# Performance work log

Measured on AMD Instinct MI355X. Metric: run time of the kernel, lower is better.

## Reference

```python
import jax, jax.numpy as jnp
import numpy as np

HIDDEN = 1024
HEADS = 12
HEAD_DIM = 64
NEG = -1e12


def _rope(x):
    # x: [B, N, H, d], rotate along seq axis (axis 1), interleaved pairs
    B, N, H, d = x.shape
    inv_freq = 1.0 / (10000.0 ** (jnp.arange(0, d, 2, dtype=jnp.float32) / d))  # [d/2]
    pos = jnp.arange(N, dtype=jnp.float32)
    ang = pos[:, None] * inv_freq[None, :]                 # [N, d/2]
    sin = jnp.repeat(jnp.sin(ang), 2, axis=-1)[None, :, None, :]  # [1,N,1,d]
    cos = jnp.repeat(jnp.cos(ang), 2, axis=-1)[None, :, None, :]
    even = x[..., ::2]
    odd = x[..., 1::2]
    rot = jnp.stack([-odd, even], axis=-1).reshape(B, N, H, d)
    return x * cos + rot * sin


def setup_inputs() -> dict:
    key = jax.random.key(0)
    k1, k2, k3, k4 = jax.random.split(key, 4)
    hidden_states = jax.random.normal(k1, (16, 512, HIDDEN), dtype=jnp.float32)
    attention_weights = jax.random.randint(k2, (16, 512), 0, 2, dtype=jnp.int32)
    W = jax.random.normal(k3, (HIDDEN, HEADS * HEAD_DIM * 2), dtype=jnp.float32) * 0.02
    b = jax.random.normal(k4, (HEADS * HEAD_DIM * 2,), dtype=jnp.float32) * 0.02
    return {"hidden_states": hidden_states, "attention_weights": attention_weights, "W": W, "b": b}


def reference(hidden_states, attention_weights, W, b):
    B, N, _ = hidden_states.shape
    proj = hidden_states @ W + b                            # [B,N,H*2*d]
    proj = proj.reshape(B, N, HEADS, 2, HEAD_DIM)
    q, k = proj[..., 0, :], proj[..., 1, :]                 # [B,N,H,d]
    q = _rope(q)
    k = _rope(k)
    q = q / (HEAD_DIM ** 0.5)
    scores = jnp.einsum('bnhd,bmhd->bhnm', q, k)            # [B,H,N,N]
    # mask padded keys (key dim only, matching the torch repeat pattern)
    key_mask = (attention_weights == 0)[:, None, None, :]   # [B,1,1,N]
    scores = jnp.where(key_mask, NEG, scores)
    # mask diagonal
    diag = jnp.eye(N, dtype=bool)[None, None, :, :]
    scores = jnp.where(diag, NEG, scores)
    return jax.nn.sigmoid(scores)
```

## Files before the change

### kernel.cpp

```cpp
#include <hip/hip_runtime.h>

#define HEADS 12
#define HIDDEN 1024
#define NOUT 1536
#define SEQ 512

typedef __bf16 bf16x8 __attribute__((ext_vector_type(8)));
typedef float f32x4 __attribute__((ext_vector_type(4)));

__device__ __forceinline__ void gload_lds16(const void* g, void* l) {
  __builtin_amdgcn_global_load_lds(
      (const __attribute__((address_space(1))) unsigned int*)g,
      (__attribute__((address_space(3))) unsigned int*)l, 16, 0, 0);
}

__device__ __forceinline__ unsigned short f2bf(float f) {
  union { float f; unsigned u; } x;
  x.f = f;
  unsigned r = x.u + 0x7fffu + ((x.u >> 16) & 1u);
  return (unsigned short)(r >> 16);
}

__device__ __forceinline__ int swz8(int b, int per) {
  return (b & 7) * per + (b >> 3);
}

__global__ __launch_bounds__(256) void k_prep(const float* __restrict__ hidden,
                                              unsigned short* __restrict__ hidA,
                                              const float* __restrict__ W,
                                              unsigned short* __restrict__ Wt,
                                              float2* __restrict__ trig) {
  __shared__ unsigned short t[32][33];
  const int bid = blockIdx.x;
  const int tid = threadIdx.x;
  if (bid < 8192) {
    int i = bid * 256 + tid;
    float4 v = ((const float4*)hidden)[i];
    ushort4 o;
    o.x = f2bf(v.x); o.y = f2bf(v.y); o.z = f2bf(v.z); o.w = f2bf(v.w);
    ((ushort4*)hidA)[i] = o;
  } else if (bid < 8192 + 1536) {
    int tt = bid - 8192;
    int n0 = (tt % 48) * 32;
    int k0 = (tt / 48) * 32;
    int tx = tid & 31;
    int ty = tid >> 5;
#pragma unroll
    for (int i = 0; i < 4; ++i) {
      int k = k0 + ty + i * 8;
      t[ty + i * 8][tx] = f2bf(W[(size_t)k * NOUT + n0 + tx]);
    }
    __syncthreads();
#pragma unroll
    for (int i = 0; i < 4; ++i) {
      int n = n0 + ty + i * 8;
      Wt[(size_t)n * HIDDEN + k0 + tx] = t[tx][ty + i * 8];
    }
  } else {
    int i = (bid - 9728) * 256 + tid;
    int pos = i >> 5, j = i & 31;
    float inv = 1.0f / powf(10000.0f, (float)(2 * j) * (1.0f / 64.0f));
    float ang = (float)pos * inv;
    trig[i] = make_float2(cosf(ang), sinf(ang));
  }
}

__global__ __launch_bounds__(256) void k_proj(const unsigned short* __restrict__ A,
                                              const unsigned short* __restrict__ Bt,
                                              const float* __restrict__ bias,
                                              const float2* __restrict__ trig,
                                              unsigned short* __restrict__ qb,
                                              unsigned short* __restrict__ kb) {
  __shared__ unsigned short As[128 * 64];
  __shared__ unsigned short Bs[128 * 64];
  const int lin = swz8(blockIdx.x, 96);
  const int h = lin % 12;
  const int m0 = (lin / 12) * 128;
  const int n0 = h * 128;
  const int tid = threadIdx.x;
  const int wave = tid >> 6, lane = tid & 63;
  const int l15 = lane & 15, l4 = lane >> 4;
  const int wr = wave >> 1, wc = wave & 1;

  f32x4 acc[4][4];
#pragma unroll
  for (int a = 0; a < 4; ++a)
#pragma unroll
    for (int b2 = 0; b2 < 4; ++b2) acc[a][b2] = (f32x4){0.f, 0.f, 0.f, 0.f};

  for (int kt = 0; kt < 16; ++kt) {
    __syncthreads();
    const int kbase = kt * 64;
#pragma unroll
    for (int i = 0; i < 4; ++i) {
      int chunk = i * 256 + tid;
      int r = chunk >> 3, c8 = chunk & 7;
      gload_lds16(A + (size_t)(m0 + r) * HIDDEN + kbase + c8 * 8, As + chunk * 8);
      gload_lds16(Bt + (size_t)(n0 + r) * HIDDEN + kbase + c8 * 8, Bs + chunk * 8);
    }
    asm volatile("s_waitcnt vmcnt(0)" ::: "memory");
    __syncthreads();
#pragma unroll
    for (int kk = 0; kk < 2; ++kk) {
      bf16x8 af[4], bv[4];
#pragma unroll
      for (int mi = 0; mi < 4; ++mi)
        af[mi] = *(const bf16x8*)(As + (wr * 64 + mi * 16 + l15) * 64 + kk * 32 + l4 * 8);
#pragma unroll
      for (int ni = 0; ni < 4; ++ni)
        bv[ni] = *(const bf16x8*)(Bs + (wc * 64 + ni * 16 + l15) * 64 + kk * 32 + l4 * 8);
#pragma unroll
      for (int mi = 0; mi < 4; ++mi)
#pragma unroll
        for (int ni = 0; ni < 4; ++ni)
          acc[mi][ni] = __builtin_amdgcn_mfma_f32_16x16x32_bf16(af[mi], bv[ni], acc[mi][ni], 0, 0, 0);
    }
  }

#pragma unroll
  for (int ni = 0; ni < 4; ++ni) {
    const int c = wc * 64 + ni * 16 + l15;
    const int qk = c >> 6;
    const int d = c & 63;
    const int j = d >> 1;
    const int odd = d & 1;
    const float bias_v = bias[n0 + c];
    unsigned short* dst = qk ? kb : qb;
    const float scale = qk ? 1.0f : 0.125f;
#pragma unroll
    for (int mi = 0; mi < 4; ++mi) {
#pragma unroll
      for (int jj = 0; jj < 4; ++jj) {
        const int row = wr * 64 + mi * 16 + l4 * 4 + jj;
        const int m = m0 + row;
        const int bb = m >> 9, pos = m & 511;
        float v = acc[mi][ni][jj] + bias_v;
        float p = __shfl_xor(v, 1);
        float2 cs = trig[pos * 32 + j];
        float o = odd ? (v * cs.x + p * cs.y) : (v * cs.x - p * cs.y);
        o *= scale;
        dst[(((size_t)bb * HEADS + h) * SEQ + pos) * 64 + d] = f2bf(o);
      }
    }
  }
}

__global__ __launch_bounds__(256) void k_scores(const unsigned short* __restrict__ qb,
                                                const unsigned short* __restrict__ kb,
                                                const int* __restrict__ aw,
                                                float* __restrict__ out) {
  __shared__ unsigned short Qs[128 * 64];
  __shared__ unsigned short Ks[2][128 * 64];
  const int lin = swz8(blockIdx.x, 96);
  const int bh = lin >> 2;
  const int b = bh / HEADS;
  const int q0 = (lin & 3) * 128;
  const int tid = threadIdx.x;
  const int wave = tid >> 6, lane = tid & 63;
  const int l15 = lane & 15, l4 = lane >> 4;
  const int wr = wave >> 1, wc = wave & 1;

  const unsigned short* qsrc = qb + (size_t)bh * SEQ * 64 + (size_t)q0 * 64;
  const unsigned short* ksrc = kb + (size_t)bh * SEQ * 64;

#pragma unroll
  for (int i = 0; i < 4; ++i) {
    int chunk = i * 256 + tid;
    gload_lds16(qsrc + chunk * 8, Qs + chunk * 8);
    gload_lds16(ksrc + chunk * 8, &Ks[0][chunk * 8]);
  }
  asm volatile("s_waitcnt vmcnt(0)" ::: "memory");
  __syncthreads();

  for (int tk = 0; tk < 4; ++tk) {
    const int cur = tk & 1;
    const int k0 = tk * 128;

    if (tk < 3) {
      const unsigned short* nsrc = ksrc + (size_t)(k0 + 128) * 64;
#pragma unroll
      for (int i = 0; i < 4; ++i) {
        int chunk = i * 256 + tid;
        gload_lds16(nsrc + chunk * 8, &Ks[cur ^ 1][chunk * 8]);
      }
    }

    f32x4 acc[4][4];
#pragma unroll
    for (int a = 0; a < 4; ++a)
#pragma unroll
      for (int b2 = 0; b2 < 4; ++b2) acc[a][b2] = (f32x4){0.f, 0.f, 0.f, 0.f};

#pragma unroll
    for (int kk = 0; kk < 2; ++kk) {
      bf16x8 qf[4], kf[4];
#pragma unroll
      for (int mi = 0; mi < 4; ++mi)
        qf[mi] = *(const bf16x8*)(Qs + (wr * 64 + mi * 16 + l15) * 64 + kk * 32 + l4 * 8);
#pragma unroll
      for (int ni = 0; ni < 4; ++ni)
        kf[ni] = *(const bf16x8*)(&Ks[cur][0] + (wc * 64 + ni * 16 + l15) * 64 + kk * 32 + l4 * 8);
#pragma unroll
      for (int mi = 0; mi < 4; ++mi)
#pragma unroll
        for (int ni = 0; ni < 4; ++ni)
          acc[mi][ni] = __builtin_amdgcn_mfma_f32_16x16x32_bf16(qf[mi], kf[ni], acc[mi][ni], 0, 0, 0);
    }

#pragma unroll
    for (int ni = 0; ni < 4; ++ni) {
      const int c = wc * 64 + ni * 16 + l15;
      const int key = k0 + c;
      const int awv = aw[b * SEQ + key];
#pragma unroll
      for (int mi = 0; mi < 4; ++mi) {
#pragma unroll
        for (int jj = 0; jj < 4; ++jj) {
          const int row = wr * 64 + mi * 16 + l4 * 4 + jj;
          const int nq = q0 + row;
          float s = acc[mi][ni][jj];
          float o = (awv == 0 || nq == key) ? 0.0f : 1.0f / (1.0f + __expf(-s));
          out[((size_t)bh * SEQ + nq) * SEQ + key] = o;
        }
      }
    }

    __syncthreads();
  }
}

extern "C" void kernel_launch(void* const* d_in, const int* in_sizes, int n_in,
                              void* d_out, int out_size, void* d_ws, size_t ws_size,
                              hipStream_t stream) {
  const float* hidden = (const float*)d_in[0];
  const int* aw = (const int*)d_in[1];
  const float* W = (const float*)d_in[2];
  const float* bias = (const float*)d_in[3];
  float* out = (float*)d_out;

  char* ws = (char*)d_ws;
  unsigned short* hidA = (unsigned short*)ws;
  unsigned short* Wt = (unsigned short*)(ws + 16777216);
  unsigned short* qb = (unsigned short*)(ws + 19922944);
  unsigned short* kb = (unsigned short*)(ws + 32505856);
  float2* trig = (float2*)(ws + 45088768);

  k_prep<<<9792, 256, 0, stream>>>(hidden, hidA, W, Wt, trig);
  k_proj<<<768, 256, 0, stream>>>(hidA, Wt, bias, trig, qb, kb);
  k_scores<<<768, 256, 0, stream>>>(qb, kb, aw, out);
}
```

Baseline: 122.8 us.

## Triple-buffer projection GEMM with swizzled LDS and async prefetch

Restructures the k_proj GEMM main loop to use K-tiles of 32 with a three-stage LDS ring buffer. Global-to-LDS loads run two tiles ahead, and partial vmcnt waits replace the full drain on every iteration. LDS chunks are XOR-swizzled to avoid bank conflicts, and MFMA sections are wrapped in s_setprio. The aim is to overlap memory latency with matrix math, at the cost of more barriers per K and tighter occupancy hints.

```diff
diff --git a/kernel.cpp b/kernel.cpp
--- a/kernel.cpp
+++ b/kernel.cpp
@@ -65,14 +65,14 @@
   }
 }
 
-__global__ __launch_bounds__(256) void k_proj(const unsigned short* __restrict__ A,
-                                              const unsigned short* __restrict__ Bt,
-                                              const float* __restrict__ bias,
-                                              const float2* __restrict__ trig,
-                                              unsigned short* __restrict__ qb,
-                                              unsigned short* __restrict__ kb) {
-  __shared__ unsigned short As[128 * 64];
-  __shared__ unsigned short Bs[128 * 64];
+__global__ __launch_bounds__(256, 3) void k_proj(const unsigned short* __restrict__ A,
+                                                 const unsigned short* __restrict__ Bt,
+                                                 const float* __restrict__ bias,
+                                                 const float2* __restrict__ trig,
+                                                 unsigned short* __restrict__ qb,
+                                                 unsigned short* __restrict__ kb) {
+  __shared__ unsigned short As[3][128 * 32];
+  __shared__ unsigned short Bs[3][128 * 32];
   const int lin = swz8(blockIdx.x, 96);
   const int h = lin % 12;
   const int m0 = (lin / 12) * 128;
@@ -81,6 +81,16 @@
   const int wave = tid >> 6, lane = tid & 63;
   const int l15 = lane & 15, l4 = lane >> 4;
   const int wr = wave >> 1, wc = wave & 1;
+  const int cchunk = (l4 ^ ((l15 >> 1) & 3)) * 8;
+
+  const int c0 = tid, c1 = 256 + tid;
+  const int r0 = c0 >> 2, r1 = c1 >> 2;
+  const int s0 = ((c0 & 3) ^ ((r0 >> 1) & 3)) * 8;
+  const int s1 = ((c1 & 3) ^ ((r1 >> 1) & 3)) * 8;
+  const unsigned short* A0 = A + (size_t)(m0 + r0) * HIDDEN + s0;
+  const unsigned short* A1 = A + (size_t)(m0 + r1) * HIDDEN + s1;
+  const unsigned short* B0 = Bt + (size_t)(n0 + r0) * HIDDEN + s0;
+  const unsigned short* B1 = Bt + (size_t)(n0 + r1) * HIDDEN + s1;
 
   f32x4 acc[4][4];
 #pragma unroll
@@ -88,34 +98,46 @@
 #pragma unroll
     for (int b2 = 0; b2 < 4; ++b2) acc[a][b2] = (f32x4){0.f, 0.f, 0.f, 0.f};
 
-  for (int kt = 0; kt < 16; ++kt) {
-    __syncthreads();
-    const int kbase = kt * 64;
-#pragma unroll
-    for (int i = 0; i < 4; ++i) {
-      int chunk = i * 256 + tid;
-      int r = chunk >> 3, c8 = chunk & 7;
-      gload_lds16(A + (size_t)(m0 + r) * HIDDEN + kbase + c8 * 8, As + chunk * 8);
-      gload_lds16(Bt + (size_t)(n0 + r) * HIDDEN + kbase + c8 * 8, Bs + chunk * 8);
-    }
-    asm volatile("s_waitcnt vmcnt(0)" ::: "memory");
-    __syncthreads();
-#pragma unroll
-    for (int kk = 0; kk < 2; ++kk) {
-      bf16x8 af[4], bv[4];
-#pragma unroll
-      for (int mi = 0; mi < 4; ++mi)
-        af[mi] = *(const bf16x8*)(As + (wr * 64 + mi * 16 + l15) * 64 + kk * 32 + l4 * 8);
-#pragma unroll
-      for (int ni = 0; ni < 4; ++ni)
-        bv[ni] = *(const bf16x8*)(Bs + (wc * 64 + ni * 16 + l15) * 64 + kk * 32 + l4 * 8);
-#pragma unroll
-      for (int mi = 0; mi < 4; ++mi)
-#pragma unroll
-        for (int ni = 0; ni < 4; ++ni)
-          acc[mi][ni] = __builtin_amdgcn_mfma_f32_16x16x32_bf16(af[mi], bv[ni], acc[mi][ni], 0, 0, 0);
-    }
-  }
+#define STAGE(KT, BUF) do {                                   \
+    const int kb_ = (KT) * 32;                                \
+    gload_lds16(A0 + kb_, &As[BUF][c0 * 8]);                  \
+    gload_lds16(A1 + kb_, &As[BUF][c1 * 8]);                  \
+    gload_lds16(B0 + kb_, &Bs[BUF][c0 * 8]);                  \
+    gload_lds16(B1 + kb_, &Bs[BUF][c1 * 8]);                  \
+  } while (0)
+
+#define STEP(KT, CUR, STG, DO_STAGE, VMC) do {                                         \
+    if (DO_STAGE) STAGE((KT) + 2, STG);                                                \
+    asm volatile("s_waitcnt vmcnt(" #VMC ")" ::: "memory");                            \
+    __builtin_amdgcn_s_barrier();                                                      \
+    bf16x8 af[4], bv[4];                                                               \
+    const unsigned short* Ab_ = &As[CUR][0];                                           \
+    const unsigned short* Bb_ = &Bs[CUR][0];                                           \
+    _Pragma("unroll") for (int mi = 0; mi < 4; ++mi)                                   \
+      af[mi] = *(const bf16x8*)(Ab_ + (wr * 64 + mi * 16 + l15) * 32 + cchunk);        \
+    _Pragma("unroll") for (int ni = 0; ni < 4; ++ni)                                   \
+      bv[ni] = *(const bf16x8*)(Bb_ + (wc * 64 + ni * 16 + l15) * 32 + cchunk);        \
+    __builtin_amdgcn_s_setprio(1);                                                     \
+    _Pragma("unroll") for (int mi = 0; mi < 4; ++mi)                                   \
+      _Pragma("unroll") for (int ni = 0; ni < 4; ++ni)                                 \
+        acc[mi][ni] = __builtin_amdgcn_mfma_f32_16x16x32_bf16(af[mi], bv[ni],          \
+                                                              acc[mi][ni], 0, 0, 0);   \
+    __builtin_amdgcn_s_setprio(0);                                                     \
+    asm volatile("s_waitcnt lgkmcnt(0)" ::: "memory");                                 \
+    __builtin_amdgcn_s_barrier();                                                      \
+  } while (0)
+
+  STAGE(0, 0);
+  STAGE(1, 1);
+  for (int t = 0; t < 30; t += 3) {
+    STEP(t, 0, 2, true, 8);
+    STEP(t + 1, 1, 0, true, 8);
+    STEP(t + 2, 2, 1, true, 8);
+  }
+  STEP(30, 0, 0, false, 4);
+  STEP(31, 1, 0, false, 0);
+#undef STEP
+#undef STAGE
 
 #pragma unroll
   for (int ni = 0; ni < 4; ++ni) {
```

New measurement: 105.4 us. -14.2%, faster.
